# Optimization experiments

Measured on AMD Instinct MI355X. Metric: run time of the kernel, lower is better.

The kernel has to match this reference:

```python
import jax, jax.numpy as jnp
import numpy as np
from jax import lax

DIM = 192
PATCH = 8


def conv1x1(x, w):
    # x: [b,c,h,w], w: [o,c] (1x1 conv, no bias)
    return jnp.einsum('bchw,oc->bohw', x, w)


def dwconv(x, w, b, pad):
    # depthwise conv, w: [C,1,kh,kw], groups = C
    y = lax.conv_general_dilated(
        x, w, window_strides=(1, 1), padding=((pad, pad), (pad, pad)),
        dimension_numbers=('NCHW', 'OIHW', 'NCHW'),
        feature_group_count=x.shape[1])
    return y + b[None, :, None, None]


def to_patches(x, p):
    b, c, h, w = x.shape
    ph = (-h) % p
    pw = (-w) % p
    x = jnp.pad(x, ((0, 0), (0, 0), (0, ph), (0, pw)))
    H, W = h + ph, w + pw
    x = x.reshape(b, c, H // p, p, W // p, p)
    return x.transpose(0, 1, 2, 4, 3, 5)  # b c nh nw p p


def from_patches(x, h, w):
    b, c, nh, nw, p, _ = x.shape
    x = x.transpose(0, 1, 2, 4, 3, 5).reshape(b, c, nh * p, nw * p)
    return x[:, :, :h, :w]


def setup_inputs() -> dict:
    key = jax.random.key(0)
    ks = jax.random.split(key, 8)
    b, c, h, w = 4, DIM, 256, 256
    x = jax.random.normal(ks[0], (b, c, h, w), jnp.float32)
    wq = jax.random.normal(ks[1], (c, c), jnp.float32) * 0.02
    w_qdw = jax.random.normal(ks[2], (c, 1, 3, 3), jnp.float32) * 0.1
    b_qdw = jnp.zeros((c,), jnp.float32)
    wkv = jax.random.normal(ks[3], (2 * c, c), jnp.float32) * 0.02
    w_kvdw = jax.random.normal(ks[4], (2 * c, 1, 7, 7), jnp.float32) * 0.05
    b_kvdw = jnp.zeros((2 * c,), jnp.float32)
    ln_w = jnp.ones((c,), jnp.float32)
    ln_b = jnp.zeros((c,), jnp.float32)
    w_proj = jax.random.normal(ks[5], (c, c), jnp.float32) * 0.02
    b_proj = jnp.zeros((c,), jnp.float32)
    return {'x': x, 'wq': wq, 'w_qdw': w_qdw, 'b_qdw': b_qdw,
            'wkv': wkv, 'w_kvdw': w_kvdw, 'b_kvdw': b_kvdw,
            'ln_w': ln_w, 'ln_b': ln_b, 'w_proj': w_proj, 'b_proj': b_proj}


def reference(x, wq, w_qdw, b_qdw, wkv, w_kvdw, b_kvdw, ln_w, ln_b, w_proj, b_proj):
    b, c, h, w = x.shape
    p = PATCH
    q = dwconv(conv1x1(x, wq), w_qdw, b_qdw, pad=1)
    kv = dwconv(conv1x1(x, wkv), w_kvdw, b_kvdw, pad=3)
    k, v = kv[:, :c], kv[:, c:]
    qp = to_patches(q, p).astype(jnp.float32)
    kp = to_patches(k, p).astype(jnp.float32)
    out = jnp.fft.irfft2(jnp.fft.rfft2(qp) * jnp.fft.rfft2(kp), s=(p, p))
    out = from_patches(out, h, w)
    # WithBias LayerNorm over channel dim (channels-last LN in original)
    mu = out.mean(axis=1, keepdims=True)
    var = out.var(axis=1, keepdims=True)
    out = (out - mu) / jnp.sqrt(var + 1e-5)
    out = out * ln_w[None, :, None, None] + ln_b[None, :, None, None]
    out = out * v
    out = conv1x1(out, w_proj) + b_proj[None, :, None, None]
    return out
```

## Files before the change

### kernel.cpp

```cpp
#include <hip/hip_runtime.h>
#include <hip/hip_bf16.h>

#define HW 65536
#define IMG 256
static constexpr int CDIM = 192;

typedef __attribute__((ext_vector_type(8))) short short8;
typedef __attribute__((ext_vector_type(4))) short s16x4;
typedef __attribute__((ext_vector_type(4))) float f32x4;

static __device__ __forceinline__ float b2f(unsigned short u) {
    union { unsigned u; float f; } t; t.u = ((unsigned)u) << 16; return t.f;
}
static __device__ __forceinline__ unsigned short f2bu(float f) {
    __hip_bfloat16 h = __float2bfloat16(f);
    return *reinterpret_cast<unsigned short*>(&h);
}

__global__ void pack_weights(const float* __restrict__ wq,
                             const float* __restrict__ wkv,
                             const float* __restrict__ wp,
                             __hip_bfloat16* __restrict__ Wqkv,
                             __hip_bfloat16* __restrict__ Wp) {
    int i = blockIdx.x * 256 + threadIdx.x;
    if (i < 36864) Wqkv[i] = __float2bfloat16(wq[i]);
    else if (i < 110592) Wqkv[i] = __float2bfloat16(wkv[i - 36864]);
    else if (i < 147456) Wp[i - 110592] = __float2bfloat16(wp[i - 110592]);
}

__global__ void gemm_bf16_x(const __hip_bfloat16* __restrict__ A,
                            const float* __restrict__ X,
                            __hip_bfloat16* __restrict__ Y) {
    __shared__ short Bs[128][200];
    const int tid = threadIdx.x;
    const int wid = tid >> 6, lane = tid & 63;
    const int mBase = blockIdx.x * 64, nBase = blockIdx.y * 128;
    const int px = tid & 127, h = tid >> 7;

#pragma unroll 4
    for (int l = 0; l < 48; l++) {
        int c = h * 96 + l * 2;
        float a = X[(size_t)c * HW + nBase + px];
        float b = X[(size_t)(c + 1) * HW + nBase + px];
        *(unsigned*)&Bs[px][c] = (unsigned)f2bu(a) | ((unsigned)f2bu(b) << 16);
    }
    __syncthreads();

    const int lr = lane & 15, lg = lane >> 4;
    const __hip_bfloat16* Ab = A + (size_t)(mBase + wid * 16 + lr) * 192 + lg * 8;
    f32x4 acc[8];
#pragma unroll
    for (int f = 0; f < 8; f++) acc[f] = (f32x4){0.f, 0.f, 0.f, 0.f};

#pragma unroll
    for (int ks = 0; ks < 6; ks++) {
        short8 af = *(const short8*)(Ab + ks * 32);
#pragma unroll
        for (int f = 0; f < 8; f++) {
            short8 bfr = *(const short8*)&Bs[f * 16 + lr][ks * 32 + lg * 8];
            acc[f] = __builtin_amdgcn_mfma_f32_16x16x32_bf16(af, bfr, acc[f], 0, 0, 0);
        }
    }

    const int mrow = mBase + wid * 16 + lg * 4;
#pragma unroll
    for (int f = 0; f < 8; f++) {
        int n = nBase + f * 16 + lr;
#pragma unroll
        for (int r = 0; r < 4; r++)
            Y[(size_t)(mrow + r) * HW + n] = __float2bfloat16(acc[f][r]);
    }
}

__global__ __launch_bounds__(256) void dwconv7_v4(
    const __hip_bfloat16* __restrict__ in,
    const float* __restrict__ wdw,
    const float* __restrict__ bias,
    __hip_bfloat16* __restrict__ out) {
    __shared__ unsigned short tile[70][136];
    const int c = blockIdx.y;
    const int x0 = (blockIdx.x & 1) * 128;
    const int y0 = (blockIdx.x >> 1) * 64;
    const __hip_bfloat16* src = in + (size_t)c * HW;

    float w49[49];
#pragma unroll
    for (int i = 0; i < 49; i++) w49[i] = wdw[c * 49 + i];
    const float bval = bias[c];

#pragma unroll
    for (int l = 0; l < 5; l++) {
        int idx = threadIdx.x + l * 256;
        if (idx < 70 * 17) {
            int r = idx / 17, cs = idx - r * 17;
            int gy = y0 + r - 3;
            int gxb = x0 + cs * 8 - 3;
            if ((unsigned)gy < IMG && gxb >= 0 && gxb + 8 <= IMG) {
                *(short8*)&tile[r][cs * 8] =
                    *(const short8*)(src + gy * IMG + gxb);
            } else {
#pragma unroll
                for (int e = 0; e < 8; e++) {
                    int gx = gxb + e;
                    unsigned short val = 0;
                    if ((unsigned)gy < IMG && (unsigned)gx < IMG)
                        val = *(const unsigned short*)(src + gy * IMG + gx);
                    tile[r][cs * 8 + e] = val;
                }
            }
        }
    }
    __syncthreads();

    const int tx4 = (threadIdx.x & 31) * 4;
    const int gy8 = (threadIdx.x >> 5) * 8;
    float acc[8][4];
#pragma unroll
    for (int j = 0; j < 8; j++)
#pragma unroll
        for (int xx = 0; xx < 4; xx++) acc[j][xx] = bval;

#pragma unroll
    for (int rr = 0; rr < 14; rr++) {
        const unsigned short* rowp = &tile[gy8 + rr][tx4];
        s16x4 a0 = *(const s16x4*)(rowp);
        s16x4 a1 = *(const s16x4*)(rowp + 4);
        s16x4 a2 = *(const s16x4*)(rowp + 8);
        float win[12];
#pragma unroll
        for (int e = 0; e < 4; e++) {
            win[e]     = b2f((unsigned short)a0[e]);
            win[e + 4] = b2f((unsigned short)a1[e]);
            win[e + 8] = b2f((unsigned short)a2[e]);
        }
#pragma unroll
        for (int j = 0; j < 8; j++) {
            const int ky = rr - j;
            if (ky >= 0 && ky < 7) {
#pragma unroll
                for (int kx = 0; kx < 7; kx++)
#pragma unroll
                    for (int xx = 0; xx < 4; xx++)
                        acc[j][xx] += win[xx + kx] * w49[ky * 7 + kx];
            }
        }
    }

    __hip_bfloat16* dst = out + (size_t)c * HW + (size_t)(y0 + gy8) * IMG + x0 + tx4;
#pragma unroll
    for (int j = 0; j < 8; j++) {
        union { unsigned short h[4]; unsigned long long u; } ob;
#pragma unroll
        for (int xx = 0; xx < 4; xx++) ob.h[xx] = f2bu(acc[j][xx]);
        *(unsigned long long*)(dst + (size_t)j * IMG) = ob.u;
    }
}

__global__ __launch_bounds__(256) void circ_qfused(
    const __hip_bfloat16* __restrict__ q0,
    const __hip_bfloat16* __restrict__ kbuf,
    const float* __restrict__ w_qdw, const float* __restrict__ b_qdw,
    __hip_bfloat16* __restrict__ sout) {
    __shared__ float qs[10][264];
    __shared__ float qP[32][68];
    __shared__ float kP[32][68];
    const int c = blockIdx.y, ph = blockIdx.x;
    const int y0 = ph * 8;
    const __hip_bfloat16* qsrc = q0 + (size_t)c * HW;
    const __hip_bfloat16* ksrc = kbuf + (size_t)c * HW;

    for (int t = threadIdx.x; t < 340; t += 256) {
        if (t < 320) {
            int r = t >> 5, ch = t & 31;
            int gy = y0 + r - 1;
            f32x4 lo = (f32x4){0.f, 0.f, 0.f, 0.f};
            f32x4 hi = (f32x4){0.f, 0.f, 0.f, 0.f};
            if ((unsigned)gy < IMG) {
                short8 v = *(const short8*)(qsrc + gy * IMG + ch * 8);
#pragma unroll
                for (int e = 0; e < 4; e++) {
                    lo[e] = b2f((unsigned short)v[e]);
                    hi[e] = b2f((unsigned short)v[4 + e]);
                }
            }
            *(f32x4*)&qs[r][4 + ch * 8] = lo;
            *(f32x4*)&qs[r][8 + ch * 8] = hi;
        } else {
            int e = t - 320;
            int r = e >> 1, s = e & 1;
            qs[r][s ? 260 : 3] = 0.f;
        }
    }
    {
        int a = threadIdx.x >> 5, ch = threadIdx.x & 31;
        short8 v = *(const short8*)(ksrc + (y0 + a) * IMG + ch * 8);
        f32x4 lo, hi;
#pragma unroll
        for (int e = 0; e < 4; e++) {
            lo[e] = b2f((unsigned short)v[e]);
            hi[e] = b2f((unsigned short)v[4 + e]);
        }
        *(f32x4*)&kP[ch][a * 8] = lo;
        *(f32x4*)&kP[ch][a * 8 + 4] = hi;
    }
    __syncthreads();

    {
        const int x = threadIdx.x;
        float w9[9];
#pragma unroll
        for (int i = 0; i < 9; i++) w9[i] = w_qdw[c * 9 + i];
        float accq[8];
#pragma unroll
        for (int j = 0; j < 8; j++) accq[j] = b_qdw[c];
#pragma unroll
        for (int kx = 0; kx < 3; kx++)
#pragma unroll
            for (int yy = 0; yy < 10; yy++) {
                float vv = qs[yy][x + kx + 3];
#pragma unroll
                for (int j = 0; j < 8; j++) {
                    int ky = yy - j;
                    if (ky >= 0 && ky < 3) accq[j] += vv * w9[ky * 3 + kx];
                }
            }
#pragma unroll
        for (int j = 0; j < 8; j++) qP[x >> 3][j * 8 + (x & 7)] = accq[j];
    }
    __syncthreads();

    const int i = threadIdx.x >> 5, pw = threadIdx.x & 31;
    float qv[8][8];
#pragma unroll
    for (int a = 0; a < 8; a++) {
        f32x4 u0 = *(const f32x4*)&qP[pw][a * 8];
        f32x4 u1 = *(const f32x4*)&qP[pw][a * 8 + 4];
        qv[a][0] = u0[0]; qv[a][1] = u0[1]; qv[a][2] = u0[2]; qv[a][3] = u0[3];
        qv[a][4] = u1[0]; qv[a][5] = u1[1]; qv[a][6] = u1[2]; qv[a][7] = u1[3];
    }
    float acc[8];
#pragma unroll
    for (int j = 0; j < 8; j++) acc[j] = 0.f;
#pragma unroll
    for (int a = 0; a < 8; a++) {
        const int r = (i - a + 8) & 7;
        f32x4 k0v = *(const f32x4*)&kP[pw][r * 8];
        f32x4 k1v = *(const f32x4*)&kP[pw][r * 8 + 4];
        float kr[8] = {k0v[0], k0v[1], k0v[2], k0v[3],
                       k1v[0], k1v[1], k1v[2], k1v[3]};
#pragma unroll
        for (int b = 0; b < 8; b++)
#pragma unroll
            for (int j = 0; j < 8; j++)
                acc[j] += qv[a][b] * kr[(j - b + 8) & 7];
    }
    union { unsigned short h[8]; short8 s8; } ob;
#pragma unroll
    for (int j = 0; j < 8; j++) ob.h[j] = f2bu(acc[j]);
    *(short8*)(sout + (size_t)c * HW + (size_t)(y0 + i) * IMG + pw * 8) = ob.s8;
}

__global__ __launch_bounds__(256, 2) void gemm_proj_ln(
    const __hip_bfloat16* __restrict__ Wp,
    const __hip_bfloat16* __restrict__ s,
    const __hip_bfloat16* __restrict__ v,
    const float* __restrict__ ln_w, const float* __restrict__ ln_b,
    const float* __restrict__ bias,
    float* __restrict__ Y) {
    __shared__ short Bs[128][200];
    __shared__ float red[2][2][128];
    __shared__ float muA[128], rsA[128];
    const int tid = threadIdx.x;
    const int p0 = blockIdx.x * 128;
    const int px = tid & 127, h = tid >> 7;
    const unsigned short* sp = (const unsigned short*)s;

    float sum = 0.f, sq = 0.f;
#pragma unroll 4
    for (int l = 0; l < 48; l++) {
        int c = h * 96 + l * 2;
        unsigned short ua = sp[(size_t)c * HW + p0 + px];
        unsigned short ub = sp[(size_t)(c + 1) * HW + p0 + px];
        float a = b2f(ua), b = b2f(ub);
        sum += a + b;
        sq += a * a + b * b;
        *(unsigned*)&Bs[px][c] = (unsigned)ua | ((unsigned)ub << 16);
    }
    red[h][0][px] = sum;
    red[h][1][px] = sq;
    __syncthreads();
    if (tid < 128) {
        float sm = red[0][0][tid] + red[1][0][tid];
        float sQ = red[0][1][tid] + red[1][1][tid];
        float mu = sm * (1.f / 192.f);
        float var = sQ * (1.f / 192.f) - mu * mu;
        muA[tid] = mu;
        rsA[tid] = rsqrtf(var + 1e-5f);
    }
    __syncthreads();

    const float mu = muA[px], rs = rsA[px];
#pragma unroll 4
    for (int l = 0; l < 48; l++) {
        int c = h * 96 + l * 2;
        unsigned pr = *(unsigned*)&Bs[px][c];
        float a = b2f((unsigned short)pr);
        float b = b2f((unsigned short)(pr >> 16));
        float va = b2f(*(const unsigned short*)(v + (size_t)c * HW + p0 + px));
        float vb = b2f(*(const unsigned short*)(v + (size_t)(c + 1) * HW + p0 + px));
        a = ((a - mu) * rs * ln_w[c] + ln_b[c]) * va;
        b = ((b - mu) * rs * ln_w[c + 1] + ln_b[c + 1]) * vb;
        *(unsigned*)&Bs[px][c] = (unsigned)f2bu(a) | ((unsigned)f2bu(b) << 16);
    }
    __syncthreads();

    const int wid = tid >> 6, lane = tid & 63;
    const int lr = lane & 15, lg = lane >> 4;
    f32x4 acc[3][8];
#pragma unroll
    for (int mf = 0; mf < 3; mf++)
#pragma unroll
        for (int f = 0; f < 8; f++) acc[mf][f] = (f32x4){0.f, 0.f, 0.f, 0.f};

#pragma unroll
    for (int ks = 0; ks < 6; ks++) {
        short8 bfr[8];
#pragma unroll
        for (int f = 0; f < 8; f++)
            bfr[f] = *(const short8*)&Bs[f * 16 + lr][ks * 32 + lg * 8];
#pragma unroll
        for (int mf = 0; mf < 3; mf++) {
            int mrow = wid * 48 + mf * 16 + lr;
            short8 af = *(const short8*)(Wp + (size_t)mrow * 192 + ks * 32 + lg * 8);
#pragma unroll
            for (int f = 0; f < 8; f++)
                acc[mf][f] = __builtin_amdgcn_mfma_f32_16x16x32_bf16(af, bfr[f], acc[mf][f], 0, 0, 0);
        }
    }

#pragma unroll
    for (int mf = 0; mf < 3; mf++) {
        int m0 = wid * 48 + mf * 16 + lg * 4;
#pragma unroll
        for (int f = 0; f < 8; f++) {
            int n = p0 + f * 16 + lr;
#pragma unroll
            for (int r = 0; r < 4; r++)
                Y[(size_t)(m0 + r) * HW + n] = acc[mf][f][r] + bias[m0 + r];
        }
    }
}

extern "C" void kernel_launch(void* const* d_in, const int* in_sizes, int n_in,
                              void* d_out, int out_size, void* d_ws, size_t ws_size,
                              hipStream_t stream) {
    const float* x      = (const float*)d_in[0];
    const float* wq     = (const float*)d_in[1];
    const float* w_qdw  = (const float*)d_in[2];
    const float* b_qdw  = (const float*)d_in[3];
    const float* wkv    = (const float*)d_in[4];
    const float* w_kvdw = (const float*)d_in[5];
    const float* b_kvdw = (const float*)d_in[6];
    const float* ln_w   = (const float*)d_in[7];
    const float* ln_b   = (const float*)d_in[8];
    const float* w_proj = (const float*)d_in[9];
    const float* b_proj = (const float*)d_in[10];
    float* out = (float*)d_out;
    char* ws = (char*)d_ws;

    __hip_bfloat16* qkv0  = (__hip_bfloat16*)(ws + 0);
    __hip_bfloat16* kvbuf = (__hip_bfloat16*)(ws + 75497472ull);
    __hip_bfloat16* sbuf  = (__hip_bfloat16*)(ws + 125829120ull);
    __hip_bfloat16* Wqkv  = (__hip_bfloat16*)(ws + 150994944ull);
    __hip_bfloat16* Wp    = Wqkv + 110592;

    pack_weights<<<576, 256, 0, stream>>>(wq, wkv, w_proj, Wqkv, Wp);

    for (int b = 0; b < 4; b++) {
        const float* xb = x + (size_t)b * CDIM * HW;
        gemm_bf16_x<<<dim3(9, HW / 128), 256, 0, stream>>>(Wqkv, xb, qkv0);
        dwconv7_v4<<<dim3(8, 384), 256, 0, stream>>>(qkv0 + (size_t)192 * HW,
                                                     w_kvdw, b_kvdw, kvbuf);
        circ_qfused<<<dim3(32, 192), 256, 0, stream>>>(qkv0, kvbuf,
                                                       w_qdw, b_qdw, sbuf);
        gemm_proj_ln<<<HW / 128, 256, 0, stream>>>(Wp, sbuf,
                                                   kvbuf + (size_t)192 * HW,
                                                   ln_w, ln_b, b_proj,
                                                   out + (size_t)b * CDIM * HW);
    }
}
```

Before: 727.5 us.

## Pre-transpose input to bf16 pixel-major and vectorize dwconv7 with packed float2 FMAs

Adds a transpose-and-convert kernel that writes x as bf16 in pixel-major layout. The QKV GEMM can then load its B tile with wide 16-byte copies instead of re-reading and converting the fp32 input in each of the 9 M-blocks. The 7x7 depthwise conv now accumulates in float2 vectors so the compiler can emit packed FMA instructions. This costs an extra kernel launch and a round trip through a bf16 intermediate buffer in exchange for less redundant global traffic and fewer ALU instructions.

```diff
diff --git a/kernel.cpp b/kernel.cpp
--- a/kernel.cpp
+++ b/kernel.cpp
@@ -8,6 +8,7 @@
 typedef __attribute__((ext_vector_type(8))) short short8;
 typedef __attribute__((ext_vector_type(4))) short s16x4;
 typedef __attribute__((ext_vector_type(4))) float f32x4;
+typedef __attribute__((ext_vector_type(2))) float f32x2;
 
 static __device__ __forceinline__ float b2f(unsigned short u) {
     union { unsigned u; float f; } t; t.u = ((unsigned)u) << 16; return t.f;
@@ -28,21 +29,35 @@
     else if (i < 147456) Wp[i - 110592] = __float2bfloat16(wp[i - 110592]);
 }
 
-__global__ void gemm_bf16_x(const __hip_bfloat16* __restrict__ A,
-                            const float* __restrict__ X,
-                            __hip_bfloat16* __restrict__ Y) {
+__global__ void transpose_cvt(const float* __restrict__ x,
+                              __hip_bfloat16* __restrict__ xT) {
+    __shared__ float tile[32][33];
+    const int p0 = blockIdx.x * 32, c0 = blockIdx.y * 32;
+    const int tx = threadIdx.x & 31, ty = threadIdx.x >> 5;
+#pragma unroll
+    for (int r = 0; r < 4; r++)
+        tile[ty + r * 8][tx] = x[(size_t)(c0 + ty + r * 8) * HW + p0 + tx];
+    __syncthreads();
+#pragma unroll
+    for (int r = 0; r < 4; r++)
+        xT[(size_t)(p0 + ty + r * 8) * 192 + c0 + tx] =
+            __float2bfloat16(tile[tx][ty + r * 8]);
+}
+
+__global__ void gemm_bf16(const __hip_bfloat16* __restrict__ A,
+                          const __hip_bfloat16* __restrict__ Bt,
+                          __hip_bfloat16* __restrict__ Y) {
     __shared__ short Bs[128][200];
     const int tid = threadIdx.x;
     const int wid = tid >> 6, lane = tid & 63;
     const int mBase = blockIdx.x * 64, nBase = blockIdx.y * 128;
-    const int px = tid & 127, h = tid >> 7;
-
-#pragma unroll 4
-    for (int l = 0; l < 48; l++) {
-        int c = h * 96 + l * 2;
-        float a = X[(size_t)c * HW + nBase + px];
-        float b = X[(size_t)(c + 1) * HW + nBase + px];
-        *(unsigned*)&Bs[px][c] = (unsigned)f2bu(a) | ((unsigned)f2bu(b) << 16);
+
+#pragma unroll
+    for (int l = 0; l < 12; l++) {
+        int ch = tid + l * 256;
+        int row = ch / 24, cc = ch % 24;
+        short8 v = *(const short8*)(Bt + (size_t)(nBase + row) * 192 + cc * 8);
+        *(short8*)&Bs[row][cc * 8] = v;
     }
     __syncthreads();
 
@@ -72,7 +87,7 @@
     }
 }
 
-__global__ __launch_bounds__(256) void dwconv7_v4(
+__global__ __launch_bounds__(256) void dwconv7_v5(
     const __hip_bfloat16* __restrict__ in,
     const float* __restrict__ wdw,
     const float* __restrict__ bias,
@@ -114,11 +129,12 @@
 
     const int tx4 = (threadIdx.x & 31) * 4;
     const int gy8 = (threadIdx.x >> 5) * 8;
-    float acc[8][4];
-#pragma unroll
-    for (int j = 0; j < 8; j++)
-#pragma unroll
-        for (int xx = 0; xx < 4; xx++) acc[j][xx] = bval;
+    f32x2 acc2[8][2];
+#pragma unroll
+    for (int j = 0; j < 8; j++) {
+        acc2[j][0] = (f32x2){bval, bval};
+        acc2[j][1] = (f32x2){bval, bval};
+    }
 
 #pragma unroll
     for (int rr = 0; rr < 14; rr++) {
@@ -138,10 +154,12 @@
             const int ky = rr - j;
             if (ky >= 0 && ky < 7) {
 #pragma unroll
-                for (int kx = 0; kx < 7; kx++)
-#pragma unroll
-                    for (int xx = 0; xx < 4; xx++)
-                        acc[j][xx] += win[xx + kx] * w49[ky * 7 + kx];
+                for (int kx = 0; kx < 7; kx++) {
+                    const float w = w49[ky * 7 + kx];
+                    const f32x2 wv = (f32x2){w, w};
+                    acc2[j][0] += (f32x2){win[kx], win[kx + 1]} * wv;
+                    acc2[j][1] += (f32x2){win[kx + 2], win[kx + 3]} * wv;
+                }
             }
         }
     }
@@ -150,8 +168,10 @@
 #pragma unroll
     for (int j = 0; j < 8; j++) {
         union { unsigned short h[4]; unsigned long long u; } ob;
-#pragma unroll
-        for (int xx = 0; xx < 4; xx++) ob.h[xx] = f2bu(acc[j][xx]);
+        ob.h[0] = f2bu(acc2[j][0][0]);
+        ob.h[1] = f2bu(acc2[j][0][1]);
+        ob.h[2] = f2bu(acc2[j][1][0]);
+        ob.h[3] = f2bu(acc2[j][1][1]);
         *(unsigned long long*)(dst + (size_t)j * IMG) = ob.u;
     }
 }
@@ -371,15 +391,17 @@
     __hip_bfloat16* qkv0  = (__hip_bfloat16*)(ws + 0);
     __hip_bfloat16* kvbuf = (__hip_bfloat16*)(ws + 75497472ull);
     __hip_bfloat16* sbuf  = (__hip_bfloat16*)(ws + 125829120ull);
-    __hip_bfloat16* Wqkv  = (__hip_bfloat16*)(ws + 150994944ull);
+    __hip_bfloat16* xT    = (__hip_bfloat16*)(ws + 150994944ull);
+    __hip_bfloat16* Wqkv  = (__hip_bfloat16*)(ws + 176160768ull);
     __hip_bfloat16* Wp    = Wqkv + 110592;
 
     pack_weights<<<576, 256, 0, stream>>>(wq, wkv, w_proj, Wqkv, Wp);
 
     for (int b = 0; b < 4; b++) {
         const float* xb = x + (size_t)b * CDIM * HW;
-        gemm_bf16_x<<<dim3(9, HW / 128), 256, 0, stream>>>(Wqkv, xb, qkv0);
-        dwconv7_v4<<<dim3(8, 384), 256, 0, stream>>>(qkv0 + (size_t)192 * HW,
+        transpose_cvt<<<dim3(HW / 32, 6), 256, 0, stream>>>(xb, xT);
+        gemm_bf16<<<dim3(9, HW / 128), 256, 0, stream>>>(Wqkv, xT, qkv0);
+        dwconv7_v5<<<dim3(8, 384), 256, 0, stream>>>(qkv0 + (size_t)192 * HW,
                                                      w_kvdw, b_kvdw, kvbuf);
         circ_qfused<<<dim3(32, 192), 256, 0, stream>>>(qkv0, kvbuf,
                                                        w_qdw, b_qdw, sbuf);
```

Result: faster. 700.6 us (-3.7%).
